# Optimization experiments

Hardware: AMD Instinct MI355X
Metric: run time of the kernel (lower is better)

Reference implementation:

```python
import jax, jax.numpy as jnp
import numpy as np

NB_ATOMS = 64
NB_FREE = 8
A = 9                      # atom_size
PAD = (A - 1) // 2         # circular padding for atom convs
TOL = 1e-4
N_ITERS = 20               # fixed-length unroll of the iPALM solver
B, H, W = 4, 1, 128        # y: [B, 1, 128, 128]

DN = ('NCHW', 'OIHW', 'NCHW')


def circ_conv(x, w, pad):
    # F.conv2d(F.pad(x, circular), w)
    xp = jnp.pad(x, ((0, 0), (0, 0), (pad, pad), (pad, pad)), mode='wrap')
    return jax.lax.conv_general_dilated(xp, w, (1, 1), 'VALID', dimension_numbers=DN)


def circ_conv_t(x, w, pad):
    # F.conv2d(pad(x), w.flip(2,3).permute(1,0,2,3))  (adjoint conv, circular)
    wt = jnp.transpose(jnp.flip(w, (2, 3)), (1, 0, 2, 3))
    return circ_conv(x, wt, pad)


def bjorck(Wm, n_iter=15):
    # Bjorck orthonormalization: rows become orthonormal.
    Wm = Wm / jnp.linalg.norm(Wm, ord=2)
    def body(w, _):
        return 1.5 * w - 0.5 * (w @ (w.T @ w)), None
    Wm, _ = jax.lax.scan(body, Wm, None, length=n_iter)
    return Wm


def soft_threshold(x, lmbda):
    # L1 prox
    return jnp.sign(x) * jnp.maximum(jnp.abs(x) - lmbda, 0.0)


def _forward(y, atoms_p, free_atoms_p, beta_p, lmbda):
    dt = y.dtype
    # --- filter preprocessing -------------------------------------------
    fa = bjorck(free_atoms_p.reshape(NB_FREE, -1))                 # [F, A*A]
    gram = fa.T @ fa                                               # [A*A, A*A]
    proj = jnp.eye(A * A, dtype=dt) - gram
    proj_filters = (proj - proj.mean(axis=1)[None, :]).reshape(A * A, 1, A, A)
    dirac = jnp.zeros((1, 1, 2 * A - 1, 2 * A - 1), dt).at[0, 0, A - 1, A - 1].set(1.0)
    proj_impulse = circ_conv_t(circ_conv(dirac, proj_filters, PAD), proj_filters, PAD)  # [1,1,17,17]
    L_pk = jnp.abs(jnp.fft.fft2(proj_impulse, s=(y.shape[2], y.shape[3]))).max()
    beta = jax.nn.relu(beta_p)
    L = 1.01 * beta * L_pk

    atoms = atoms_p - atoms_p.mean(axis=(1, 2, 3), keepdims=True)
    af = atoms.reshape(NB_ATOMS, -1)
    af = af - af @ gram                                            # remove free-atom span
    af = af / jnp.linalg.norm(af, axis=1, keepdims=True)
    af = jnp.sqrt(0.99 / jnp.maximum(beta, 0.1)) * af / jnp.linalg.norm(af, ord=2)
    atoms = af.reshape(NB_ATOMS, 1, A, A)
    Xmat = af @ af.T                                               # [K, K] (1x1 conv)

    # --- iPALM fixed-point iterations -----------------------------------
    coeffs0 = jnp.zeros((y.shape[0], NB_ATOMS, y.shape[2], y.shape[3]), dt)
    active0 = jnp.ones((y.shape[0],), dtype=bool)

    def step(state, k):
        img, new_img, coeffs, new_coeffs, active = state
        m4 = active[:, None, None, None]
        kf = k.astype(dt)
        mom = (kf - 1.0) / (kf + 2.0)

        temp_c = new_coeffs + (new_coeffs - coeffs) * mom
        grad_c = jnp.einsum('oc,bchw->bohw', Xmat, temp_c) - circ_conv(new_img, atoms, PAD)
        upd_c = soft_threshold(temp_c - beta * grad_c, lmbda)
        coeffs2 = jnp.where(m4, new_coeffs, coeffs)
        new_coeffs2 = jnp.where(m4, upd_c, new_coeffs)

        temp_i = new_img + (new_img - img) * mom
        dict_pred = circ_conv_t(new_coeffs2, atoms, PAD)           # [B,1,H,W]
        sum_p = circ_conv(temp_i, proj_impulse, A - 1)             # [B,1,H,W]
        img2 = jnp.where(m4, new_img, img)
        upd_i = temp_i - (temp_i - y + beta * (sum_p - dict_pred)) / L
        new_img2 = jnp.where(m4, upd_i, new_img)

        d = img2 - new_img2
        res = jnp.sqrt(jnp.sum(d * d, axis=(1, 2, 3))) / jnp.sqrt(jnp.sum(img2 * img2, axis=(1, 2, 3)))
        return (img2, new_img2, coeffs2, new_coeffs2, res > TOL), None

    state0 = (y, y, coeffs0, coeffs0, active0)
    (img, new_img, coeffs, new_coeffs, _), _ = jax.lax.scan(
        step, state0, jnp.arange(1, N_ITERS + 1))
    return new_img, new_coeffs


def setup_inputs() -> dict:
    key = jax.random.key(0)
    k1, k2, k3 = jax.random.split(key, 3)
    y = jax.random.normal(k1, (B, H, 128, 128), dtype=jnp.float32)
    atoms = jax.random.normal(k2, (NB_ATOMS, 1, A, A), dtype=jnp.float32) / 3000.0
    free_atoms = jax.random.normal(k3, (NB_FREE, 1, A, A), dtype=jnp.float32) / 3000.0
    beta = jnp.asarray(1.0, dtype=jnp.float32)
    lmbda = jnp.asarray(1e-3, dtype=jnp.float32)
    return {"y": y, "atoms": atoms, "free_atoms": free_atoms, "beta": beta, "lmbda": lmbda}


def reference(y, atoms, free_atoms, beta, lmbda):
    return _forward(y, atoms, free_atoms, beta, lmbda)
```

## Files before the change

kernel.cpp:

```cpp
#include <hip/hip_runtime.h>
#include <math.h>


#define NB 4
#define NCH 64
#define NPIX 16384
#define NPB (NCH*NPIX)
#define NCOEF (NB*NCH*NPIX)
#define NIMG  (NB*NPIX)
#define NPG 32
#define TOLV 1e-4f

#define SC_BETA 0
#define SC_L    1
#define SC_G    4
#define SC_G2   5
#define SC_LPK2 6

__global__ __launch_bounds__(256) void k_prep1(const float* __restrict__ fatoms,
    const float* __restrict__ beta_p,
    float* __restrict__ gram_g, float* __restrict__ pf_g,
    float* __restrict__ scalars)
{
    __shared__ float sW[648], sWf[648];
    __shared__ float sG[64], sP[64], sF[64], sT[64], sTmp[64];
    __shared__ float sGr[6561];
    __shared__ float rs[81];
    __shared__ float sSig;
    int tid = threadIdx.x;
    if (tid==0){ float b=beta_p[0]; scalars[SC_BETA]=(b>0.f)?b:0.f;
                 ((unsigned*)scalars)[SC_LPK2]=0u; }
    for (int e=tid; e<648; e+=256) sW[e]=fatoms[e];
    __syncthreads();
    if (tid<64){ int r=tid>>3, s=tid&7; float a=0.f;
        for (int k=0;k<81;++k) a=fmaf(sW[r*81+k],sW[s*81+k],a); sG[tid]=a; }
    __syncthreads();
    if (tid<64){
        int r8 = tid&7;
        float v = 1.f;
        for (int it=0; it<64; ++it){
            float nv=0.f;
            #pragma unroll
            for (int j=0;j<8;++j) nv = fmaf(sG[r8*8+j], __shfl(v,j,8), nv);
            float m = fabsf(nv);
            m = fmaxf(m, __shfl_xor(m,1,8));
            m = fmaxf(m, __shfl_xor(m,2,8));
            m = fmaxf(m, __shfl_xor(m,4,8));
            v = nv/m;
        }
        float wv=0.f;
        #pragma unroll
        for (int j=0;j<8;++j) wv = fmaf(sG[r8*8+j], __shfl(v,j,8), wv);
        float num=v*wv, den=v*v;
        num += __shfl_xor(num,1,8); num += __shfl_xor(num,2,8); num += __shfl_xor(num,4,8);
        den += __shfl_xor(den,1,8); den += __shfl_xor(den,2,8); den += __shfl_xor(den,4,8);
        if (tid==0) sSig = sqrtf(num/den);
    }
    __syncthreads();
    float inv_s = 1.f/sSig;
    for (int e=tid; e<648; e+=256) sW[e]*=inv_s;
    if (tid<64){ sG[tid]*=inv_s*inv_s; sP[tid]=((tid>>3)==(tid&7))?1.f:0.f; }
    __syncthreads();
    for (int it=0; it<15; ++it){
        if (tid<64) sF[tid] = (((tid>>3)==(tid&7))?1.5f:0.f) - 0.5f*sG[tid];
        __syncthreads();
        if (tid<64){ int r=tid>>3, c=tid&7; float ap=0.f, ag=0.f;
            #pragma unroll
            for (int k=0;k<8;++k){ float f=sF[r*8+k]; ap=fmaf(f,sP[k*8+c],ap); ag=fmaf(f,sG[k*8+c],ag); }
            sTmp[tid]=ap; sT[tid]=ag; }
        __syncthreads();
        if (tid<64){ int r=tid>>3, c=tid&7; float g2=0.f;
            #pragma unroll
            for (int k=0;k<8;++k) g2=fmaf(sT[r*8+k],sF[k*8+c],g2);
            sG[tid]=g2; sP[tid]=sTmp[tid]; }
        __syncthreads();
    }
    for (int e=tid; e<648; e+=256){ int r=e/81, j=e%81; float a=0.f;
        #pragma unroll
        for (int k=0;k<8;++k) a=fmaf(sP[r*8+k], sW[k*81+j], a);
        sWf[e]=a; }
    __syncthreads();
    for (int e=tid; e<6561; e+=256){ int i=e/81, j=e%81; float a=0.f;
        #pragma unroll
        for (int r=0;r<8;++r) a=fmaf(sWf[r*81+i],sWf[r*81+j],a);
        sGr[e]=a; gram_g[e]=a; }
    __syncthreads();
    if (tid<81){ float s=0.f; for (int k=0;k<81;++k) s+=sGr[tid*81+k]; rs[tid]=(1.f-s)/81.f; }
    __syncthreads();
    for (int e=tid; e<6561; e+=256){ int i=e/81, j=e%81;
        pf_g[e] = ((i==j)?1.f:0.f) - sGr[e] - rs[j]; }
}

__global__ __launch_bounds__(256) void k_PP(const float* __restrict__ pf, float* __restrict__ PP)
{
    __shared__ float spf[6561];
    for (int e=threadIdx.x; e<6561; e+=256) spf[e]=pf[e];
    __syncthreads();
    int e = blockIdx.x*256 + threadIdx.x;
    if (e>=6561) return;
    int al=e/81, be=e%81; float a=0.f;
    for (int c=0;c<81;++c) a=fmaf(spf[c*81+al], spf[c*81+be], a);
    PP[e]=a;
}

__global__ void k_impulse(const float* __restrict__ PP, float* __restrict__ pi)
{
    int t = threadIdx.x;
    if (t>=289) return;
    int h=t/17, w=t%17;
    float acc=0.f;
    for (int p=0;p<9;++p){
        int i2=(h+p-4+17)%17;
        if (i2<4||i2>12) continue;
        for (int q=0;q<9;++q){
            int j2=(w+q-4+17)%17;
            if (j2<4||j2>12) continue;
            int al=(12-i2)*9+(12-j2);
            int be=(8-p)*9+(8-q);
            acc += PP[al*81+be];
        }
    }
    pi[t]=acc;
}

__global__ __launch_bounds__(64) void k_dft(const float* __restrict__ pi, float* __restrict__ scalars)
{
    __shared__ float spi[289], ct[128], st[128];
    int tid=threadIdx.x; int gid=blockIdx.x*64+tid;
    for (int e=tid; e<289; e+=64) spi[e]=pi[e];
    for (int e=tid; e<128; e+=64){ float ang=(float)e*(6.28318530717958647692f/128.f);
                  ct[e]=cosf(ang); st[e]=sinf(ang); }
    __syncthreads();
    int u=gid>>7, v=gid&127;
    float re=0.f, im=0.f;
    for (int i=0;i<17;++i){
        int ku=(u*i)&127;
        const float* prow=spi+i*17;
        for (int j=0;j<17;++j){
            int k=(ku+v*j)&127;
            float x=prow[j];
            re=fmaf(x,ct[k],re); im=fmaf(x,st[k],im);
        }
    }
    float m2=re*re+im*im;
    #pragma unroll
    for (int d=32; d; d>>=1) m2=fmaxf(m2, __shfl_down(m2,d));
    if (tid==0) atomicMax(((unsigned*)scalars)+SC_LPK2, __float_as_uint(m2));
}

__global__ __launch_bounds__(128) void k_atoms1(const float* __restrict__ atoms_in,
    const float* __restrict__ gram, float* __restrict__ af_rn, float* __restrict__ af_rnT)
{
    int a=blockIdx.x, tid=threadIdx.x;
    __shared__ float a0[81], a1[81], rbuf[128];
    float v = (tid<81)? atoms_in[a*81+tid] : 0.f;
    rbuf[tid]=v; __syncthreads();
    for (int off=64; off; off>>=1){ if (tid<off) rbuf[tid]+=rbuf[tid+off]; __syncthreads(); }
    float mean = rbuf[0]/81.f;
    __syncthreads();
    if (tid<81) a0[tid]=v-mean;
    __syncthreads();
    float w=0.f;
    if (tid<81){ float dot=0.f;
        for (int k=0;k<81;++k) dot=fmaf(a0[k], gram[k*81+tid], dot);
        w=a0[tid]-dot; a1[tid]=w; }
    rbuf[tid]=(tid<81)? w*w : 0.f;
    __syncthreads();
    for (int off=64; off; off>>=1){ if (tid<off) rbuf[tid]+=rbuf[tid+off]; __syncthreads(); }
    float inv = 1.f/sqrtf(rbuf[0]);
    if (tid<81){ float r=a1[tid]*inv; af_rn[a*81+tid]=r; af_rnT[tid*64+a]=r; }
}

__global__ __launch_bounds__(256) void k_M(const float* __restrict__ af_rn,
    const float* __restrict__ af_rnT, float* __restrict__ M)
{
    int e=blockIdx.x*256+threadIdx.x;
    int i=e>>6, j=e&63;
    float a=0.f;
    for (int k=0;k<81;++k) a=fmaf(af_rn[i*81+k], af_rnT[(k<<6)+j], a);
    M[e]=a;
}

__global__ __launch_bounds__(256) void k_M2(const float* __restrict__ IN,
    float* __restrict__ OUT)
{
    int e=blockIdx.x*256+threadIdx.x;
    int i=e>>6, j=e&63;
    float a=0.f;
    for (int k=0;k<64;++k) a=fmaf(IN[(i<<6)+k], IN[(k<<6)+j], a);
    OUT[e]=a;
}

__global__ __launch_bounds__(256) void k_fin(const float* __restrict__ Mg,
    const float* __restrict__ MPg, const float* __restrict__ af_rn,
    float* __restrict__ scalars,
    float* __restrict__ atoms_f, float* __restrict__ atomsT, float* __restrict__ Xmat)
{
    __shared__ float sM[4096];
    __shared__ float sGc[2];
    int tid=threadIdx.x;
    for (int e=tid; e<4096; e+=256) sM[e]=Mg[e];
    __syncthreads();
    if (tid<64){
        float m[64];
        const float4* mp = reinterpret_cast<const float4*>(MPg + (tid<<6));
        #pragma unroll
        for (int j4=0;j4<16;++j4){
            float4 v4=mp[j4];
            m[j4*4+0]=v4.x; m[j4*4+1]=v4.y; m[j4*4+2]=v4.z; m[j4*4+3]=v4.w;
        }
        float v = 1.0f + 0.01f*(float)tid;
        for (int it=0; it<8; ++it){
            float a0=0.f,a1=0.f,a2=0.f,a3=0.f;
            #pragma unroll
            for (int j=0;j<64;j+=4){
                a0=fmaf(m[j+0], __shfl(v,j+0), a0);
                a1=fmaf(m[j+1], __shfl(v,j+1), a1);
                a2=fmaf(m[j+2], __shfl(v,j+2), a2);
                a3=fmaf(m[j+3], __shfl(v,j+3), a3);
            }
            float nv=(a0+a1)+(a2+a3);
            float mx=fabsf(nv);
            #pragma unroll
            for (int d=1; d<64; d<<=1) mx=fmaxf(mx, __shfl_xor(mx,d));
            v=nv/mx;
        }
        float w0=0.f,w1=0.f,w2=0.f,w3=0.f;
        #pragma unroll
        for (int j=0;j<64;j+=4){
            w0=fmaf(sM[(tid<<6)+j+0], __shfl(v,j+0), w0);
            w1=fmaf(sM[(tid<<6)+j+1], __shfl(v,j+1), w1);
            w2=fmaf(sM[(tid<<6)+j+2], __shfl(v,j+2), w2);
            w3=fmaf(sM[(tid<<6)+j+3], __shfl(v,j+3), w3);
        }
        float wv=(w0+w1)+(w2+w3);
        float num=v*wv, den=v*v;
        #pragma unroll
        for (int d=1; d<64; d<<=1){ num+=__shfl_xor(num,d); den+=__shfl_xor(den,d); }
        if (tid==0){
            float sig = sqrtf(num/den);
            float b = scalars[SC_BETA];
            float s = sqrtf(0.99f/fmaxf(b,0.1f));
            float g = s/sig;
            scalars[SC_G]=g; scalars[SC_G2]=g*g;
            float lpk = sqrtf(__uint_as_float(((unsigned*)scalars)[SC_LPK2]));
            scalars[SC_L] = 1.01f*b*lpk;
            sGc[0]=g; sGc[1]=g*g;
        }
    }
    __syncthreads();
    float g=sGc[0], g2=sGc[1];
    for (int idx=tid; idx<5184; idx+=256){
        int a=idx/81, pq=idx-a*81;
        float v=g*af_rn[idx];
        atoms_f[idx]=v;
        atomsT[pq*64+a]=v;
    }
    for (int e=tid; e<4096; e+=256) Xmat[e]=g2*sM[e];
}

template<bool FIRST>
__global__ __launch_bounds__(512,4) void kA(const float* __restrict__ c_in,
    float* __restrict__ nc_in, const float* __restrict__ nimg,
    const float* __restrict__ Xmat, const float* __restrict__ atomsT,
    const float* __restrict__ scalars, const float* __restrict__ lmbda_p,
    const float* __restrict__ red_in,
    float* __restrict__ nc_out, float mom)
{
    int b=blockIdx.y, h0=blockIdx.x;
    int tid=threadIdx.x;
    int wv = __builtin_amdgcn_readfirstlane(tid>>6);
    int lane = tid&63;
    int co = wv*8;
    int px = lane*2;
    __shared__ float sTemp[64*128];
    __shared__ float simg[9*128];
    __shared__ float sAct;
    if (FIRST){ if (tid==0) sAct=1.f; }
    else if (tid<64){
        float sd=red_in[(b<<7)+(tid<<1)], si=red_in[(b<<7)+(tid<<1)+1];
        #pragma unroll
        for (int off=32; off; off>>=1){ sd+=__shfl_down(sd,off); si+=__shfl_down(si,off); }
        if (tid==0) sAct = (sd > TOLV*TOLV*si) ? 1.f : 0.f;
    }
    for (int e=tid; e<1152; e+=512)
        simg[e]=nimg[b*NPIX + (((h0-4+(e>>7))&127)<<7) + (e&127)];
    size_t sbase = (size_t)b*NPB + (h0<<7);
    float2 nv8[8], cv8[8];
    if (!FIRST){
        #pragma unroll
        for (int oc=0;oc<8;++oc){
            size_t a = sbase + (size_t)(co+oc)*NPIX + px;
            cv8[oc]=*reinterpret_cast<const float2*>(c_in + a);
            nv8[oc]=*reinterpret_cast<const float2*>(nc_in + a);
            float2 t;
            t.x=fmaf(mom,nv8[oc].x-cv8[oc].x,nv8[oc].x);
            t.y=fmaf(mom,nv8[oc].y-cv8[oc].y,nv8[oc].y);
            *reinterpret_cast<float2*>(sTemp + (co+oc)*128 + px) = t;
        }
    }
    __syncthreads();
    const float* Xo = Xmat + co;
    const float* Ao = atomsT + co;
    float acc[16];
    #pragma unroll
    for (int i=0;i<16;++i) acc[i]=0.f;
    if (!FIRST){
        for (int c=0;c<64;++c){
            float2 t=*reinterpret_cast<const float2*>(sTemp + c*128 + px);
            const float* Xr = Xo + (c<<6);
            #pragma unroll
            for (int oc=0;oc<8;++oc){
                float x=Xr[oc];
                acc[oc*2+0]=fmaf(x,t.x,acc[oc*2+0]);
                acc[oc*2+1]=fmaf(x,t.y,acc[oc*2+1]);
            }
        }
    }
    for (int p=0;p<9;++p){
        const float* srow = simg + p*128;
        float in10[10];
        #pragma unroll
        for (int j=0;j<10;++j) in10[j]=srow[(px-4+j)&127];
        #pragma unroll 3
        for (int q=0;q<9;++q){
            const float* Ar = Ao + ((p*9+q)<<6);
            #pragma unroll
            for (int oc=0;oc<8;++oc){
                float a=Ar[oc];
                acc[oc*2+0]=fmaf(a,-in10[q+0],acc[oc*2+0]);
                acc[oc*2+1]=fmaf(a,-in10[q+1],acc[oc*2+1]);
            }
        }
    }
    float beta=scalars[SC_BETA], lmb=lmbda_p[0];
    bool act = (sAct!=0.f);
    #pragma unroll
    for (int oc=0;oc<8;++oc){
        size_t a = sbase + (size_t)(co+oc)*NPIX + px;
        float2 nv, cv;
        if (FIRST){ nv=make_float2(0.f,0.f); cv=nv; }
        else { nv=nv8[oc]; cv=cv8[oc]; }
        float2 nw;
        {
            float t=FIRST?0.f:fmaf(mom,nv.x-cv.x,nv.x);
            float u=fmaf(-beta,acc[oc*2+0],t); float au=fabsf(u)-lmb;
            u=(au>0.f)?copysignf(au,u):0.f; nw.x=act?u:nv.x;
        }{
            float t=FIRST?0.f:fmaf(mom,nv.y-cv.y,nv.y);
            float u=fmaf(-beta,acc[oc*2+1],t); float au=fabsf(u)-lmb;
            u=(au>0.f)?copysignf(au,u):0.f; nw.y=act?u:nv.y;
        }
        *reinterpret_cast<float2*>(nc_out + a) = nw;
        if (FIRST){
            *reinterpret_cast<float2*>(nc_in + a) = make_float2(0.f,0.f);
        } else if (!act){
            *reinterpret_cast<float2*>(nc_in + a) = cv;
        }
    }
}

__global__ __launch_bounds__(256,4) void kB1(const float* __restrict__ nc2,
    const float* __restrict__ atoms_f, float* __restrict__ part)
{
    int b=blockIdx.z, cg=blockIdx.y, pb=blockIdx.x;
    int t=threadIdx.x;
    int row = pb*16 + (t>>4);
    int cb  = (t&15)*8;
    const float* src = nc2 + (b*NCH + cg*2)*NPIX;
    float acc[8];
    #pragma unroll
    for (int k=0;k<8;++k) acc[k]=0.f;
    for (int c=0;c<2;++c){
        const float* chan = src + c*NPIX;
        const float* arow = atoms_f + (cg*2+c)*81;
        #pragma unroll 3
        for (int p=0;p<9;++p){
            int r=(row+4-p)&127;
            const float* rp_ = chan + (r<<7);
            float in16[16];
            #pragma unroll
            for (int k4=0;k4<4;++k4){
                int col=(cb-4+(k4<<2))&127;
                const float4 vv = *reinterpret_cast<const float4*>(rp_+col);
                in16[(k4<<2)+0]=vv.x; in16[(k4<<2)+1]=vv.y;
                in16[(k4<<2)+2]=vv.z; in16[(k4<<2)+3]=vv.w;
            }
            #pragma unroll
            for (int q=0;q<9;++q){
                float a = arow[p*9+q];
                #pragma unroll
                for (int k=0;k<8;++k) acc[k]=fmaf(in16[k+8-q], a, acc[k]);
            }
        }
    }
    float* dst = part + (cg*NB+b)*NPIX + (row<<7) + cb;
    #pragma unroll
    for (int k=0;k<8;++k) dst[k]=acc[k];
}

template<bool FIRST>
__global__ __launch_bounds__(512) void kB2(const float* __restrict__ img,
    const float* __restrict__ nimg, const float* __restrict__ y,
    const float* __restrict__ part, const float* __restrict__ pi,
    const float* __restrict__ scalars, const float* __restrict__ red_in,
    float* __restrict__ img_out, float* __restrict__ nimg_out,
    float* __restrict__ red_out, float mom)
{
    int b=blockIdx.y, rp=blockIdx.x;
    int tid=threadIdx.x;
    int half=tid>>8, lid=tid&255;
    int ty=lid>>7, w=lid&127;
    int h0=rp*2;
    __shared__ float sti[18*128];
    __shared__ float spi[289];
    __shared__ float sP2[256];
    __shared__ float rsd[4], rsi[4];
    __shared__ float sAct;
    if (FIRST){ if (tid==0) sAct=1.f; }
    else if (tid<64){
        float sd=red_in[(b<<7)+(tid<<1)], si=red_in[(b<<7)+(tid<<1)+1];
        #pragma unroll
        for (int off=32; off; off>>=1){ sd+=__shfl_down(sd,off); si+=__shfl_down(si,off); }
        if (tid==0) sAct = (sd > TOLV*TOLV*si) ? 1.f : 0.f;
    }
    const float* ib  = img  + b*NPIX;
    const float* nib = nimg + b*NPIX;
    for (int e=tid; e<2304; e+=512){
        int r=e>>7, cc=e&127;
        int idx=(((h0-8+r)&127)<<7)+cc;
        float nv=nib[idx], v=ib[idx];
        sti[e]=fmaf(mom, nv-v, nv);
    }
    for (int e=tid; e<289; e+=512) spi[e]=pi[e];
    __syncthreads();
    float sp=0.f;
    int pn = 9 - half;
    for (int pk=0; pk<pn; ++pk){
        int p = half*9 + pk;
        const float* srow = sti + (ty+p)*128;
        const float* pr = spi + p*17;
        #pragma unroll
        for (int q=0;q<17;++q) sp=fmaf(srow[(w+q-8)&127], pr[q], sp);
    }
    if (half==1) sP2[lid]=sp;
    __syncthreads();
    if (tid<256){
        sp += sP2[lid];
        int pix=((h0+ty)<<7)+w;
        float dp=0.f;
        #pragma unroll
        for (int g=0; g<NPG; ++g) dp += part[(g*NB+b)*NPIX + pix];
        float ti = sti[(ty+8)*128 + w];
        float beta=scalars[SC_BETA], L=scalars[SC_L];
        float yv=y[b*NPIX+pix];
        float upd = ti - (ti - yv + beta*(sp - dp))/L;
        bool act = (sAct!=0.f);
        float iv=ib[pix], niv=nib[pix];
        float i2 = act? niv : iv;
        float ni2 = act? upd : niv;
        img_out[b*NPIX+pix]=i2;
        nimg_out[b*NPIX+pix]=ni2;
        float d=i2-ni2;
        float sd=d*d, si=i2*i2;
        #pragma unroll
        for (int off=32; off; off>>=1){ sd+=__shfl_down(sd,off); si+=__shfl_down(si,off); }
        if ((tid&63)==0){ rsd[tid>>6]=sd; rsi[tid>>6]=si; }
    }
    __syncthreads();
    if (tid==0){
        float a=rsd[0]+rsd[1]+rsd[2]+rsd[3];
        float c2=rsi[0]+rsi[1]+rsi[2]+rsi[3];
        red_out[(b<<7)+(rp<<1)+0]=a;
        red_out[(b<<7)+(rp<<1)+1]=c2;
    }
}

extern "C" void kernel_launch(void* const* d_in, const int* in_sizes, int n_in,
                              void* d_out, int out_size, void* d_ws, size_t ws_size,
                              hipStream_t stream)
{
    const float* y        = (const float*)d_in[0];
    const float* atoms_p  = (const float*)d_in[1];
    const float* fatoms_p = (const float*)d_in[2];
    const float* beta_p   = (const float*)d_in[3];
    const float* lmbda_p  = (const float*)d_in[4];
    float* out = (float*)d_out;
    float* w = (float*)d_ws;

    size_t off=0;
    float* cf[3];  cf[0]=w+off; off+=NCOEF; cf[1]=w+off; off+=NCOEF; cf[2]=w+off; off+=NCOEF;
    float* ib[2];  ib[0]=w+off;  off+=NIMG;  ib[1]=w+off;  off+=NIMG;
    float* nib[2]; nib[0]=w+off; off+=NIMG;  nib[1]=w+off; off+=NIMG;
    float* part=w+off;    off+=NPG*NIMG;
    float* red[2]; red[0]=w+off; off+=512; red[1]=w+off; off+=512;
    float* gram=w+off;    off+=6561;
    float* pf=w+off;      off+=6561;
    float* PP=w+off;      off+=6561;
    float* pi=w+off;      off+=512;
    float* af_rn=w+off;   off+=5184;
    float* af_rnT=w+off;  off+=5184;
    float* Mmat=w+off;    off+=4096;
    float* MA=w+off;      off+=4096;
    float* MB=w+off;      off+=4096;
    float* atoms_f=w+off; off+=5184;
    float* atomsT=w+off;  off+=5184;
    float* Xmat=w+off;    off+=4096;
    float* scalars=w+off; off+=32;

    k_prep1<<<dim3(1),dim3(256),0,stream>>>(fatoms_p, beta_p, gram, pf, scalars);
    k_PP<<<dim3(26),dim3(256),0,stream>>>(pf, PP);
    k_impulse<<<dim3(1),dim3(320),0,stream>>>(PP, pi);
    k_dft<<<dim3(256),dim3(64),0,stream>>>(pi, scalars);
    k_atoms1<<<dim3(64),dim3(128),0,stream>>>(atoms_p, gram, af_rn, af_rnT);
    k_M<<<dim3(16),dim3(256),0,stream>>>(af_rn, af_rnT, Mmat);
    k_M2<<<dim3(16),dim3(256),0,stream>>>(Mmat, MA);
    k_M2<<<dim3(16),dim3(256),0,stream>>>(MA, MB);
    k_M2<<<dim3(16),dim3(256),0,stream>>>(MB, MA);
    k_M2<<<dim3(16),dim3(256),0,stream>>>(MA, MB);
    k_fin<<<dim3(1),dim3(256),0,stream>>>(Mmat, MB, af_rn, scalars, atoms_f, atomsT, Xmat);

    int ic=0, in=1, io=2;
    int p=0;
    for (int k=1; k<=20; ++k){
        float mom = (float)(k-1)/(float)(k+2);
        const float* rin = red[(k-1)&1];
        float* rout = red[k&1];
        const float* img_i  = (k==1)? y : ib[p];
        const float* nimg_i = (k==1)? y : nib[p];
        float* nc_t  = (k==20)? (out+NIMG) : cf[io];
        float* nimg_t= (k==20)? out : nib[p^1];
        if (k==1){
            kA<true><<<dim3(128,4),dim3(512),0,stream>>>(cf[ic],cf[in],nimg_i,Xmat,atomsT,
                scalars,lmbda_p,rin, nc_t,mom);
        } else {
            kA<false><<<dim3(128,4),dim3(512),0,stream>>>(cf[ic],cf[in],nimg_i,Xmat,atomsT,
                scalars,lmbda_p,rin, nc_t,mom);
        }
        kB1<<<dim3(8,32,4),dim3(256),0,stream>>>(nc_t, atoms_f, part);
        if (k==1){
            kB2<true><<<dim3(64,4),dim3(512),0,stream>>>(img_i,nimg_i,y,part,pi,scalars,rin,
                ib[p^1],nimg_t,rout,mom);
        } else {
            kB2<false><<<dim3(64,4),dim3(512),0,stream>>>(img_i,nimg_i,y,part,pi,scalars,rin,
                ib[p^1],nimg_t,rout,mom);
        }
        int t=ic; ic=in; in=io; io=t;
        p^=1;
    }
}
```

Before: 1.160 ms.

## Restructure atom synthesis conv to reuse rows across outputs and reduce channels in-wave

The per-channel-pair synthesis convolution is rebuilt so each thread computes a 4-row by 8-column output tile for one channel. Each input row it loads is reused across several output rows, and the 16 channels of a group are summed with sub-wave shuffles, so the partial-sum buffer drops from 32 groups to 4. Atoms are stored in a padded, float4-aligned layout written by the finalize kernel. The aim is less redundant input loading and less partial-sum traffic into kB2. In exchange, each thread holds more accumulators, so register pressure rises, and the shuffle reduction adds instructions.

```diff
diff --git a/kernel.cpp b/kernel.cpp
--- a/kernel.cpp
+++ b/kernel.cpp
@@ -8,7 +8,7 @@
 #define NPB (NCH*NPIX)
 #define NCOEF (NB*NCH*NPIX)
 #define NIMG  (NB*NPIX)
-#define NPG 32
+#define NPG 4
 #define TOLV 1e-4f
 
 #define SC_BETA 0
@@ -194,12 +194,14 @@
 __global__ __launch_bounds__(256) void k_fin(const float* __restrict__ Mg,
     const float* __restrict__ MPg, const float* __restrict__ af_rn,
     float* __restrict__ scalars,
-    float* __restrict__ atoms_f, float* __restrict__ atomsT, float* __restrict__ Xmat)
+    float* __restrict__ atoms_f, float* __restrict__ atomsT,
+    float* __restrict__ atomsP, float* __restrict__ Xmat)
 {
     __shared__ float sM[4096];
     __shared__ float sGc[2];
     int tid=threadIdx.x;
     for (int e=tid; e<4096; e+=256) sM[e]=Mg[e];
+    for (int e=tid; e<64*112; e+=256) atomsP[e]=0.f;
     __syncthreads();
     if (tid<64){
         float m[64];
@@ -255,6 +257,7 @@
         float v=g*af_rn[idx];
         atoms_f[idx]=v;
         atomsT[pq*64+a]=v;
+        atomsP[a*112 + (pq/9)*12 + (pq%9)] = v;
     }
     for (int e=tid; e<4096; e+=256) Xmat[e]=g2*sM[e];
 }
@@ -360,43 +363,75 @@
     }
 }
 
-__global__ __launch_bounds__(256,4) void kB1(const float* __restrict__ nc2,
-    const float* __restrict__ atoms_f, float* __restrict__ part)
-{
-    int b=blockIdx.z, cg=blockIdx.y, pb=blockIdx.x;
+__global__ __launch_bounds__(256) void kB1(const float* __restrict__ nc2,
+    const float* __restrict__ atomsP, float* __restrict__ part)
+{
+    int b=blockIdx.z, cgp=blockIdx.y, rb=blockIdx.x;
     int t=threadIdx.x;
-    int row = pb*16 + (t>>4);
-    int cb  = (t&15)*8;
-    const float* src = nc2 + (b*NCH + cg*2)*NPIX;
-    float acc[8];
+    int chl = t & 15;
+    int cs  = t >> 4;
+    int ch  = cgp*16 + chl;
+    int r0  = rb*4;
+    int cb  = cs*8;
+    const float* chan = nc2 + (b*NCH + ch)*NPIX;
+    const float* arowP = atomsP + ch*112;
+    float acc[4][8];
     #pragma unroll
-    for (int k=0;k<8;++k) acc[k]=0.f;
-    for (int c=0;c<2;++c){
-        const float* chan = src + c*NPIX;
-        const float* arow = atoms_f + (cg*2+c)*81;
-        #pragma unroll 3
-        for (int p=0;p<9;++p){
-            int r=(row+4-p)&127;
-            const float* rp_ = chan + (r<<7);
-            float in16[16];
-            #pragma unroll
-            for (int k4=0;k4<4;++k4){
-                int col=(cb-4+(k4<<2))&127;
-                const float4 vv = *reinterpret_cast<const float4*>(rp_+col);
-                in16[(k4<<2)+0]=vv.x; in16[(k4<<2)+1]=vv.y;
-                in16[(k4<<2)+2]=vv.z; in16[(k4<<2)+3]=vv.w;
+    for (int i=0;i<4;++i){
+        #pragma unroll
+        for (int j=0;j<8;++j) acc[i][j]=0.f;
+    }
+    for (int ir=0; ir<12; ++ir){
+        int riabs = (r0 - 4 + ir) & 127;
+        const float* rp_ = chan + (riabs<<7);
+        float in16[16];
+        #pragma unroll
+        for (int k4=0;k4<4;++k4){
+            int col=(cb-4+(k4<<2))&127;
+            const float4 vv = *reinterpret_cast<const float4*>(rp_+col);
+            in16[(k4<<2)+0]=vv.x; in16[(k4<<2)+1]=vv.y;
+            in16[(k4<<2)+2]=vv.z; in16[(k4<<2)+3]=vv.w;
+        }
+        #pragma unroll
+        for (int orr=0; orr<4; ++orr){
+            int p = orr + 8 - ir;
+            if (p>=0 && p<=8){
+                const float4* cp4 = reinterpret_cast<const float4*>(arowP + p*12);
+                float4 ca=cp4[0], cb4=cp4[1], cc=cp4[2];
+                float c9[9];
+                c9[0]=ca.x; c9[1]=ca.y; c9[2]=ca.z; c9[3]=ca.w;
+                c9[4]=cb4.x; c9[5]=cb4.y; c9[6]=cb4.z; c9[7]=cb4.w;
+                c9[8]=cc.x;
+                #pragma unroll
+                for (int q=0;q<9;++q){
+                    float a=c9[q];
+                    #pragma unroll
+                    for (int k=0;k<8;++k)
+                        acc[orr][k]=fmaf(in16[k+8-q], a, acc[orr][k]);
+                }
             }
-            #pragma unroll
-            for (int q=0;q<9;++q){
-                float a = arow[p*9+q];
-                #pragma unroll
-                for (int k=0;k<8;++k) acc[k]=fmaf(in16[k+8-q], a, acc[k]);
-            }
-        }
-    }
-    float* dst = part + (cg*NB+b)*NPIX + (row<<7) + cb;
+        }
+    }
     #pragma unroll
-    for (int k=0;k<8;++k) dst[k]=acc[k];
+    for (int i=0;i<4;++i){
+        #pragma unroll
+        for (int j=0;j<8;++j){
+            float v=acc[i][j];
+            v += __shfl_xor(v, 1, 16);
+            v += __shfl_xor(v, 2, 16);
+            v += __shfl_xor(v, 4, 16);
+            v += __shfl_xor(v, 8, 16);
+            acc[i][j]=v;
+        }
+    }
+    if (chl==0){
+        float* dst = part + (cgp*NB+b)*NPIX + (r0<<7) + cb;
+        #pragma unroll
+        for (int i=0;i<4;++i){
+            #pragma unroll
+            for (int j=0;j<8;++j) dst[(i<<7)+j]=acc[i][j];
+        }
+    }
 }
 
 template<bool FIRST>
@@ -505,6 +540,7 @@
     float* MB=w+off;      off+=4096;
     float* atoms_f=w+off; off+=5184;
     float* atomsT=w+off;  off+=5184;
+    float* atomsP=w+off;  off+=64*112;
     float* Xmat=w+off;    off+=4096;
     float* scalars=w+off; off+=32;
 
@@ -518,7 +554,7 @@
     k_M2<<<dim3(16),dim3(256),0,stream>>>(MA, MB);
     k_M2<<<dim3(16),dim3(256),0,stream>>>(MB, MA);
     k_M2<<<dim3(16),dim3(256),0,stream>>>(MA, MB);
-    k_fin<<<dim3(1),dim3(256),0,stream>>>(Mmat, MB, af_rn, scalars, atoms_f, atomsT, Xmat);
+    k_fin<<<dim3(1),dim3(256),0,stream>>>(Mmat, MB, af_rn, scalars, atoms_f, atomsT, atomsP, Xmat);
 
     int ic=0, in=1, io=2;
     int p=0;
@@ -537,7 +573,7 @@
             kA<false><<<dim3(128,4),dim3(512),0,stream>>>(cf[ic],cf[in],nimg_i,Xmat,atomsT,
                 scalars,lmbda_p,rin, nc_t,mom);
         }
-        kB1<<<dim3(8,32,4),dim3(256),0,stream>>>(nc_t, atoms_f, part);
+        kB1<<<dim3(32,4,4),dim3(256),0,stream>>>(nc_t, atomsP, part);
         if (k==1){
             kB2<true><<<dim3(64,4),dim3(512),0,stream>>>(img_i,nimg_i,y,part,pi,scalars,rin,
                 ib[p^1],nimg_t,rout,mom);
```

New measurement: 1.469 ms. 26.6% more time.
